# Kernel optimization log

Hardware: AMD Instinct MI355X
Metric: run time of the kernel (lower is better)

Reference implementation:

```python
import jax, jax.numpy as jnp
import numpy as np

N = 100000
E = 3200000
D_IN = 128
D_OUT = 128
ALPHA = 0.2  # LeakyReLU negative slope
LN_EPS = 1e-5


def setup_inputs() -> dict:
    key = jax.random.key(0)
    k1, k2, k3, k4, k5 = jax.random.split(key, 5)
    x = jax.random.normal(k1, (N, D_IN), dtype=jnp.float32)
    edge = jax.random.randint(k2, (2, E), 0, N, dtype=jnp.int64)
    # Linear params (kaiming-normal-ish init)
    W = jax.random.normal(k3, (D_OUT, D_IN), dtype=jnp.float32) * np.sqrt(2.0 / D_IN)
    b = jnp.zeros((D_OUT,), dtype=jnp.float32)
    # attention vector a: (2*out,)
    a = jax.random.normal(k4, (2 * D_OUT,), dtype=jnp.float32) * np.sqrt(2.0 / (2 * D_OUT))
    ln_w = jnp.ones((D_OUT,), dtype=jnp.float32)
    ln_b = jnp.zeros((D_OUT,), dtype=jnp.float32)
    return {"x": x, "W": W, "b": b, "a": a, "ln_w": ln_w, "ln_b": ln_b, "edge": edge}


def reference(x, W, b, a, ln_w, ln_b, edge):
    n = x.shape[0]
    d_out = W.shape[0]
    h = x @ W.T + b  # [N, D_OUT]
    src, dst = edge[0], edge[1]
    # a.mm(cat(h[src], h[dst]).T) == h[src] @ a1 + h[dst] @ a2
    a1, a2 = a[:d_out], a[d_out:]
    node_s1 = h @ a1  # [N]
    node_s2 = h @ a2  # [N]
    z = node_s1[src] + node_s2[dst]  # [E]
    edge_e = jnp.exp(-jax.nn.leaky_relu(z, ALPHA))  # [E]
    # sparse spmm: h_prime[i] = sum_{e: src=i} edge_e[e] * h[dst[e]]
    msgs = edge_e[:, None] * h[dst]  # [E, D_OUT]
    h_prime = jax.ops.segment_sum(msgs, src, num_segments=n)  # [N, D_OUT]
    # LayerNorm over last dim
    mu = jnp.mean(h_prime, axis=-1, keepdims=True)
    var = jnp.mean(jnp.square(h_prime - mu), axis=-1, keepdims=True)
    h_norm = (h_prime - mu) * jax.lax.rsqrt(var + LN_EPS) * ln_w + ln_b
    return jax.nn.elu(h_norm)
```

## Files before the change

### kernel.cpp

```cpp
#include <hip/hip_runtime.h>
#include <math.h>

#define D 128
#define GAT_ALPHA 0.2f
#define LN_EPS 1e-5f
#define NBMAX 400
#define CAP 9216
#define ECHUNK 4096

typedef __attribute__((ext_vector_type(8))) short short8;
typedef __attribute__((ext_vector_type(4))) float floatx4;

__device__ __forceinline__ unsigned short f2bf(float f) {
    unsigned u = __float_as_uint(f);
    unsigned r = (u + 0x7fffu + ((u >> 16) & 1u)) >> 16;
    return (unsigned short)r;
}
__device__ __forceinline__ float bfl(unsigned u) { return __uint_as_float(u << 16); }
__device__ __forceinline__ float bfh(unsigned u) { return __uint_as_float(u & 0xffff0000u); }

__global__ __launch_bounds__(256) void prep_bfrag(const float* __restrict__ W,
                                                  unsigned short* __restrict__ Bfrag)
{
    for (int idx = threadIdx.x; idx < 2048; idx += 256) {
        int lane = idx & 63, ntkt = idx >> 6;
        int nt = ntkt >> 2, kt = ntkt & 3;
        int l16 = lane & 15, quad = lane >> 4;
        const float* wp = W + (size_t)(nt * 16 + l16) * D + kt * 32 + quad * 8;
        unsigned short* op = Bfrag + (size_t)idx * 8;
#pragma unroll
        for (int j = 0; j < 8; ++j) op[j] = f2bf(wp[j]);
    }
}

__global__ __launch_bounds__(256) void gemm_mfma(const float* __restrict__ x,
                                                 const unsigned short* __restrict__ Bfrag_g,
                                                 const float* __restrict__ b,
                                                 const float* __restrict__ a,
                                                 unsigned short* __restrict__ h16,
                                                 float* __restrict__ s1,
                                                 float* __restrict__ s2, int n)
{
    __shared__ unsigned short Bf[16384];
    {
        const uint2* sp = (const uint2*)Bfrag_g;
        uint2* dp = (uint2*)Bf;
        for (int i = threadIdx.x; i < 4096; i += 256) dp[i] = sp[i];
    }
    __syncthreads();

    const int lane = threadIdx.x & 63, wave = threadIdx.x >> 6;
    const int l16 = lane & 15, quad = lane >> 4;
    const int row0 = blockIdx.x * 64 + wave * 16;

    floatx4 acc[8];
#pragma unroll
    for (int nt = 0; nt < 8; ++nt) acc[nt] = (floatx4){0.f, 0.f, 0.f, 0.f};

    const int arow = row0 + l16;
    const bool aval = arow < n;
    const float* xr = x + (size_t)(aval ? arow : 0) * D;

#pragma unroll
    for (int kt = 0; kt < 4; ++kt) {
        short8 af;
        if (aval) {
            const float* p = xr + kt * 32 + quad * 8;
            float4 u0 = *(const float4*)p;
            float4 u1 = *(const float4*)(p + 4);
            af[0] = (short)f2bf(u0.x); af[1] = (short)f2bf(u0.y);
            af[2] = (short)f2bf(u0.z); af[3] = (short)f2bf(u0.w);
            af[4] = (short)f2bf(u1.x); af[5] = (short)f2bf(u1.y);
            af[6] = (short)f2bf(u1.z); af[7] = (short)f2bf(u1.w);
        } else {
#pragma unroll
            for (int j = 0; j < 8; ++j) af[j] = 0;
        }
#pragma unroll
        for (int nt = 0; nt < 8; ++nt) {
            short8 bf = *(const short8*)&Bf[(size_t)((nt * 4 + kt) * 64 + lane) * 8];
            acc[nt] = __builtin_amdgcn_mfma_f32_16x16x32_bf16(af, bf, acc[nt], 0, 0, 0);
        }
    }

    float bcol[8], a1c[8], a2c[8];
#pragma unroll
    for (int nt = 0; nt < 8; ++nt) {
        int c = nt * 16 + l16;
        bcol[nt] = b[c]; a1c[nt] = a[c]; a2c[nt] = a[D + c];
    }
#pragma unroll
    for (int r = 0; r < 4; ++r) {
        int crow = row0 + quad * 4 + r;
        float hv[8];
        float p1 = 0.f, p2 = 0.f;
#pragma unroll
        for (int nt = 0; nt < 8; ++nt) {
            float v = acc[nt][r] + bcol[nt];
            hv[nt] = v;
            p1 = fmaf(v, a1c[nt], p1);
            p2 = fmaf(v, a2c[nt], p2);
        }
#pragma unroll
        for (int off = 8; off > 0; off >>= 1) {
            p1 += __shfl_xor(p1, off);
            p2 += __shfl_xor(p2, off);
        }
        if (crow < n) {
            if (l16 == 0) { s1[crow] = p1; s2[crow] = p2; }
            unsigned short* hp = h16 + (size_t)crow * D + l16;
#pragma unroll
            for (int nt = 0; nt < 8; ++nt) hp[nt * 16] = f2bf(hv[nt]);
        }
    }
}

__global__ __launch_bounds__(256) void partition_kernel(const int* __restrict__ src,
                                                        const int* __restrict__ dst,
                                                        int* __restrict__ gcnt,
                                                        int* __restrict__ pairs,
                                                        int nE, int nb)
{
    __shared__ int cnt[NBMAX], basex[NBMAX], cnt2[NBMAX];
    int tid = threadIdx.x;
    for (int i = tid; i < nb; i += 256) { cnt[i] = 0; cnt2[i] = 0; }
    __syncthreads();
    int e0 = blockIdx.x * ECHUNK;
    int e1 = e0 + ECHUNK; if (e1 > nE) e1 = nE;
    for (int e = e0 + tid; e < e1; e += 256)
        atomicAdd(&cnt[src[e] >> 8], 1);
    __syncthreads();
    for (int i = tid; i < nb; i += 256)
        basex[i] = cnt[i] ? atomicAdd(&gcnt[i], cnt[i]) : 0;
    __syncthreads();
    for (int e = e0 + tid; e < e1; e += 256) {
        int s = src[e];
        int bb = s >> 8;
        int l = basex[bb] + atomicAdd(&cnt2[bb], 1);
        if (l < CAP) pairs[(size_t)bb * CAP + l] = ((s & 255) << 24) | dst[e];
    }
}

__global__ __launch_bounds__(256) void bucket_sort(const int* __restrict__ pairs,
                                                   const int* __restrict__ gcnt,
                                                   const float* __restrict__ s1,
                                                   const float* __restrict__ s2,
                                                   int* __restrict__ beg,
                                                   int* __restrict__ end_,
                                                   int2* __restrict__ csr, int n)
{
    __shared__ int cnt[256], excl[256], cnt2[256], wsum[4];
    int bkt = blockIdx.x, tid = threadIdx.x;
    int base = bkt * CAP;
    int m = gcnt[bkt]; if (m > CAP) m = CAP;
    cnt[tid] = 0; cnt2[tid] = 0;
    __syncthreads();
    for (int e = tid; e < m; e += 256)
        atomicAdd(&cnt[((unsigned)pairs[base + e]) >> 24], 1);
    __syncthreads();

    int lane = tid & 63, wid = tid >> 6;
    int v = cnt[tid], incl = v;
#pragma unroll
    for (int off = 1; off < 64; off <<= 1) {
        int t = __shfl_up(incl, off);
        if (lane >= off) incl += t;
    }
    if (lane == 63) wsum[wid] = incl;
    __syncthreads();
    int woff = 0;
#pragma unroll
    for (int w = 0; w < 4; ++w)
        if (w < wid) woff += wsum[w];
    int ex = woff + incl - v;
    excl[tid] = ex;
    int node = bkt * 256 + tid;
    if (node < n) { beg[node] = base + ex; end_[node] = base + ex + v; }
    __syncthreads();

    for (int e = tid; e < m; e += 256) {
        int w = pairs[base + e];
        int sl = ((unsigned)w) >> 24;
        int d = w & 0xFFFFFF;
        int s = (bkt << 8) | sl;
        float z = s1[s] + s2[d];
        float lz = z > 0.f ? z : GAT_ALPHA * z;
        float ee = __expf(-lz);
        int pos = excl[sl] + atomicAdd(&cnt2[sl], 1);
        csr[base + pos] = make_int2(d, __float_as_int(ee));
    }
}

__global__ __launch_bounds__(256) void aggregate_kernel(const unsigned short* __restrict__ h16,
                                                        const int* __restrict__ beg,
                                                        const int* __restrict__ end_,
                                                        const int2* __restrict__ csr,
                                                        const float* __restrict__ ln_w,
                                                        const float* __restrict__ ln_b,
                                                        float* __restrict__ out, int n)
{
    int node = blockIdx.x * 4 + (threadIdx.x >> 6);
    if (node >= n) return;
    int lane = threadIdx.x & 63;
    int q    = lane >> 4;
    int l16  = lane & 15;

    int e0 = beg[node], e1 = end_[node];

    float acc[8];
#pragma unroll
    for (int j = 0; j < 8; ++j) acc[j] = 0.f;

    for (int e = e0 + q; e < e1; e += 4) {
        int2 p = csr[e];
        float ee = __int_as_float(p.y);
        uint4 u = *(const uint4*)(h16 + (size_t)p.x * D + l16 * 8);
        acc[0] = fmaf(ee, bfl(u.x), acc[0]);
        acc[1] = fmaf(ee, bfh(u.x), acc[1]);
        acc[2] = fmaf(ee, bfl(u.y), acc[2]);
        acc[3] = fmaf(ee, bfh(u.y), acc[3]);
        acc[4] = fmaf(ee, bfl(u.z), acc[4]);
        acc[5] = fmaf(ee, bfh(u.z), acc[5]);
        acc[6] = fmaf(ee, bfl(u.w), acc[6]);
        acc[7] = fmaf(ee, bfh(u.w), acc[7]);
    }
#pragma unroll
    for (int j = 0; j < 8; ++j) acc[j] += __shfl_down(acc[j], 32);
#pragma unroll
    for (int j = 0; j < 8; ++j) acc[j] += __shfl_down(acc[j], 16);

    float sum = 0.f, sq = 0.f;
#pragma unroll
    for (int j = 0; j < 8; ++j) { sum += acc[j]; sq += acc[j] * acc[j]; }
#pragma unroll
    for (int off = 8; off > 0; off >>= 1) {
        sum += __shfl_xor(sum, off);
        sq  += __shfl_xor(sq, off);
    }

    if (q == 0) {
        float mu   = sum * (1.0f / 128.0f);
        float var  = sq * (1.0f / 128.0f) - mu * mu;
        float rstd = rsqrtf(var + LN_EPS);

        float4 w0 = *(const float4*)(ln_w + l16 * 8);
        float4 w1 = *(const float4*)(ln_w + l16 * 8 + 4);
        float4 b0 = *(const float4*)(ln_b + l16 * 8);
        float4 b1 = *(const float4*)(ln_b + l16 * 8 + 4);
        float y[8];
        y[0] = (acc[0] - mu) * rstd * w0.x + b0.x;
        y[1] = (acc[1] - mu) * rstd * w0.y + b0.y;
        y[2] = (acc[2] - mu) * rstd * w0.z + b0.z;
        y[3] = (acc[3] - mu) * rstd * w0.w + b0.w;
        y[4] = (acc[4] - mu) * rstd * w1.x + b1.x;
        y[5] = (acc[5] - mu) * rstd * w1.y + b1.y;
        y[6] = (acc[6] - mu) * rstd * w1.z + b1.z;
        y[7] = (acc[7] - mu) * rstd * w1.w + b1.w;
#pragma unroll
        for (int j = 0; j < 8; ++j) y[j] = y[j] > 0.f ? y[j] : expm1f(y[j]);
        float* op = out + (size_t)node * D + l16 * 8;
        *(float4*)op       = make_float4(y[0], y[1], y[2], y[3]);
        *(float4*)(op + 4) = make_float4(y[4], y[5], y[6], y[7]);
    }
}

extern "C" void kernel_launch(void* const* d_in, const int* in_sizes, int n_in,
                              void* d_out, int out_size, void* d_ws, size_t ws_size,
                              hipStream_t stream)
{
    const float* x    = (const float*)d_in[0];
    const float* W    = (const float*)d_in[1];
    const float* b    = (const float*)d_in[2];
    const float* a    = (const float*)d_in[3];
    const float* ln_w = (const float*)d_in[4];
    const float* ln_b = (const float*)d_in[5];
    const int*   edge = (const int*)d_in[6];

    const int n  = in_sizes[0] / D;
    const int nE = in_sizes[6] / 2;
    const int* src = edge;
    const int* dst = edge + nE;
    const int nb = (n + 255) >> 8;

    float* out = (float*)d_out;

    unsigned short* h16 = (unsigned short*)d_ws;
    float* s1   = (float*)(h16 + (size_t)n * D);
    float* s2   = s1 + n;
    unsigned short* Bfrag = (unsigned short*)(s2 + n);
    int* pairs  = (int*)(Bfrag + 16384);
    int2* csr   = (int2*)(pairs + (size_t)nb * CAP);
    int* beg    = (int*)(csr + (size_t)nb * CAP);
    int* end_   = beg + n;
    int* gcnt   = end_ + n;

    hipMemsetAsync(gcnt, 0, (size_t)nb * sizeof(int), stream);

    prep_bfrag      <<<1, 256, 0, stream>>>(W, Bfrag);
    gemm_mfma       <<<(n + 63) / 64, 256, 0, stream>>>(x, Bfrag, b, a, h16, s1, s2, n);
    partition_kernel<<<(nE + ECHUNK - 1) / ECHUNK, 256, 0, stream>>>(src, dst, gcnt, pairs, nE, nb);
    bucket_sort     <<<nb, 256, 0, stream>>>(pairs, gcnt, s1, s2, beg, end_, csr, n);
    aggregate_kernel<<<(n + 3) / 4, 256, 0, stream>>>(h16, beg, end_, csr, ln_w, ln_b, out, n);
}
```

Baseline: 384.9 us.

## Stage GEMM tiles through LDS, enlarge partition chunks, unroll aggregation gather

The GEMM now converts x to bf16 once into a padded LDS tile and reads MFMA A-fragments from it. It also stages the h output through LDS so h16 rows are written with coalesced 16-byte stores instead of scattered 2-byte stores. The partition kernel uses 16K-edge chunks with 512 threads, which means fewer blocks and fewer global atomics on the bucket counters. The aggregation loop processes two edges per iteration so two independent row gathers are in flight at once. The cost is more shared memory per GEMM block, which may lower occupancy, and fewer partition blocks, which gives less parallelism.

```diff
diff --git a/kernel.cpp b/kernel.cpp
--- a/kernel.cpp
+++ b/kernel.cpp
@@ -6,7 +6,8 @@
 #define LN_EPS 1e-5f
 #define NBMAX 400
 #define CAP 9216
-#define ECHUNK 4096
+#define ECHUNK 16384
+#define XPITCH 136
 
 typedef __attribute__((ext_vector_type(8))) short short8;
 typedef __attribute__((ext_vector_type(4))) float floatx4;
@@ -42,40 +43,35 @@
                                                  float* __restrict__ s2, int n)
 {
     __shared__ unsigned short Bf[16384];
+    __shared__ unsigned short xs[64 * XPITCH];
+    const int tid = threadIdx.x;
     {
         const uint2* sp = (const uint2*)Bfrag_g;
         uint2* dp = (uint2*)Bf;
-        for (int i = threadIdx.x; i < 4096; i += 256) dp[i] = sp[i];
-    }
-    __syncthreads();
-
-    const int lane = threadIdx.x & 63, wave = threadIdx.x >> 6;
+        for (int i = tid; i < 4096; i += 256) dp[i] = sp[i];
+    }
+    const int row0 = blockIdx.x * 64;
+
+    for (int i = tid; i < 2048; i += 256) {
+        int row = i >> 5, c4 = i & 31;
+        float4 v = make_float4(0.f, 0.f, 0.f, 0.f);
+        if (row0 + row < n) v = *(const float4*)(x + (size_t)(row0 + row) * D + c4 * 4);
+        ushort4 o;
+        o.x = f2bf(v.x); o.y = f2bf(v.y); o.z = f2bf(v.z); o.w = f2bf(v.w);
+        *(ushort4*)&xs[row * XPITCH + c4 * 4] = o;
+    }
+    __syncthreads();
+
+    const int lane = tid & 63, wave = tid >> 6;
     const int l16 = lane & 15, quad = lane >> 4;
-    const int row0 = blockIdx.x * 64 + wave * 16;
 
     floatx4 acc[8];
 #pragma unroll
     for (int nt = 0; nt < 8; ++nt) acc[nt] = (floatx4){0.f, 0.f, 0.f, 0.f};
 
-    const int arow = row0 + l16;
-    const bool aval = arow < n;
-    const float* xr = x + (size_t)(aval ? arow : 0) * D;
-
 #pragma unroll
     for (int kt = 0; kt < 4; ++kt) {
-        short8 af;
-        if (aval) {
-            const float* p = xr + kt * 32 + quad * 8;
-            float4 u0 = *(const float4*)p;
-            float4 u1 = *(const float4*)(p + 4);
-            af[0] = (short)f2bf(u0.x); af[1] = (short)f2bf(u0.y);
-            af[2] = (short)f2bf(u0.z); af[3] = (short)f2bf(u0.w);
-            af[4] = (short)f2bf(u1.x); af[5] = (short)f2bf(u1.y);
-            af[6] = (short)f2bf(u1.z); af[7] = (short)f2bf(u1.w);
-        } else {
-#pragma unroll
-            for (int j = 0; j < 8; ++j) af[j] = 0;
-        }
+        short8 af = *(const short8*)&xs[(wave * 16 + l16) * XPITCH + kt * 32 + quad * 8];
 #pragma unroll
         for (int nt = 0; nt < 8; ++nt) {
             short8 bf = *(const short8*)&Bf[(size_t)((nt * 4 + kt) * 64 + lane) * 8];
@@ -89,15 +85,14 @@
         int c = nt * 16 + l16;
         bcol[nt] = b[c]; a1c[nt] = a[c]; a2c[nt] = a[D + c];
     }
+    float hv[4][8];
 #pragma unroll
     for (int r = 0; r < 4; ++r) {
-        int crow = row0 + quad * 4 + r;
-        float hv[8];
         float p1 = 0.f, p2 = 0.f;
 #pragma unroll
         for (int nt = 0; nt < 8; ++nt) {
             float v = acc[nt][r] + bcol[nt];
-            hv[nt] = v;
+            hv[r][nt] = v;
             p1 = fmaf(v, a1c[nt], p1);
             p2 = fmaf(v, a2c[nt], p2);
         }
@@ -106,16 +101,27 @@
             p1 += __shfl_xor(p1, off);
             p2 += __shfl_xor(p2, off);
         }
-        if (crow < n) {
-            if (l16 == 0) { s1[crow] = p1; s2[crow] = p2; }
-            unsigned short* hp = h16 + (size_t)crow * D + l16;
-#pragma unroll
-            for (int nt = 0; nt < 8; ++nt) hp[nt * 16] = f2bf(hv[nt]);
-        }
-    }
-}
-
-__global__ __launch_bounds__(256) void partition_kernel(const int* __restrict__ src,
+        int crow = row0 + wave * 16 + quad * 4 + r;
+        if (crow < n && l16 == 0) { s1[crow] = p1; s2[crow] = p2; }
+    }
+
+    __syncthreads();
+#pragma unroll
+    for (int r = 0; r < 4; ++r)
+#pragma unroll
+        for (int nt = 0; nt < 8; ++nt)
+            xs[(wave * 16 + quad * 4 + r) * XPITCH + nt * 16 + l16] = f2bf(hv[r][nt]);
+    __syncthreads();
+
+    for (int i = tid; i < 1024; i += 256) {
+        int row = i >> 4, c = i & 15;
+        if (row0 + row < n)
+            *(uint4*)(h16 + (size_t)(row0 + row) * D + c * 8) =
+                *(const uint4*)&xs[row * XPITCH + c * 8];
+    }
+}
+
+__global__ __launch_bounds__(512) void partition_kernel(const int* __restrict__ src,
                                                         const int* __restrict__ dst,
                                                         int* __restrict__ gcnt,
                                                         int* __restrict__ pairs,
@@ -123,17 +129,17 @@
 {
     __shared__ int cnt[NBMAX], basex[NBMAX], cnt2[NBMAX];
     int tid = threadIdx.x;
-    for (int i = tid; i < nb; i += 256) { cnt[i] = 0; cnt2[i] = 0; }
+    for (int i = tid; i < nb; i += 512) { cnt[i] = 0; cnt2[i] = 0; }
     __syncthreads();
     int e0 = blockIdx.x * ECHUNK;
     int e1 = e0 + ECHUNK; if (e1 > nE) e1 = nE;
-    for (int e = e0 + tid; e < e1; e += 256)
+    for (int e = e0 + tid; e < e1; e += 512)
         atomicAdd(&cnt[src[e] >> 8], 1);
     __syncthreads();
-    for (int i = tid; i < nb; i += 256)
+    for (int i = tid; i < nb; i += 512)
         basex[i] = cnt[i] ? atomicAdd(&gcnt[i], cnt[i]) : 0;
     __syncthreads();
-    for (int e = e0 + tid; e < e1; e += 256) {
+    for (int e = e0 + tid; e < e1; e += 512) {
         int s = src[e];
         int bb = s >> 8;
         int l = basex[bb] + atomicAdd(&cnt2[bb], 1);
@@ -211,7 +217,34 @@
 #pragma unroll
     for (int j = 0; j < 8; ++j) acc[j] = 0.f;
 
-    for (int e = e0 + q; e < e1; e += 4) {
+    int e = e0 + q;
+    for (; e + 4 < e1; e += 8) {
+        int2 pa = csr[e];
+        int2 pb = csr[e + 4];
+        const uint4* gpa = (const uint4*)(h16 + (size_t)pa.x * D + l16 * 8);
+        const uint4* gpb = (const uint4*)(h16 + (size_t)pb.x * D + l16 * 8);
+        uint4 ua = *gpa;
+        uint4 ub = *gpb;
+        float ea = __int_as_float(pa.y);
+        float eb = __int_as_float(pb.y);
+        acc[0] = fmaf(ea, bfl(ua.x), acc[0]);
+        acc[1] = fmaf(ea, bfh(ua.x), acc[1]);
+        acc[2] = fmaf(ea, bfl(ua.y), acc[2]);
+        acc[3] = fmaf(ea, bfh(ua.y), acc[3]);
+        acc[4] = fmaf(ea, bfl(ua.z), acc[4]);
+        acc[5] = fmaf(ea, bfh(ua.z), acc[5]);
+        acc[6] = fmaf(ea, bfl(ua.w), acc[6]);
+        acc[7] = fmaf(ea, bfh(ua.w), acc[7]);
+        acc[0] = fmaf(eb, bfl(ub.x), acc[0]);
+        acc[1] = fmaf(eb, bfh(ub.x), acc[1]);
+        acc[2] = fmaf(eb, bfl(ub.y), acc[2]);
+        acc[3] = fmaf(eb, bfh(ub.y), acc[3]);
+        acc[4] = fmaf(eb, bfl(ub.z), acc[4]);
+        acc[5] = fmaf(eb, bfh(ub.z), acc[5]);
+        acc[6] = fmaf(eb, bfl(ub.w), acc[6]);
+        acc[7] = fmaf(eb, bfh(ub.w), acc[7]);
+    }
+    for (; e < e1; e += 4) {
         int2 p = csr[e];
         float ee = __int_as_float(p.y);
         uint4 u = *(const uint4*)(h16 + (size_t)p.x * D + l16 * 8);
@@ -298,7 +331,7 @@
 
     prep_bfrag      <<<1, 256, 0, stream>>>(W, Bfrag);
     gemm_mfma       <<<(n + 63) / 64, 256, 0, stream>>>(x, Bfrag, b, a, h16, s1, s2, n);
-    partition_kernel<<<(nE + ECHUNK - 1) / ECHUNK, 256, 0, stream>>>(src, dst, gcnt, pairs, nE, nb);
+    partition_kernel<<<(nE + ECHUNK - 1) / ECHUNK, 512, 0, stream>>>(src, dst, gcnt, pairs, nE, nb);
     bucket_sort     <<<nb, 256, 0, stream>>>(pairs, gcnt, s1, s2, beg, end_, csr, n);
     aggregate_kernel<<<(n + 3) / 4, 256, 0, stream>>>(h16, beg, end_, csr, ln_w, ln_b, out, n);
 }
```

New measurement: 362.7 us. 1.06x faster.
